# Kernel optimization log

Measured on AMD Instinct MI355X. Metric: run time of the kernel, lower is better.

## Reference

```python
import jax, jax.numpy as jnp
import numpy as np

B, T, D = 4, 2048, 1024
H, DH = 16, 64

def setup_inputs() -> dict:
    key = jax.random.key(0)
    k1, k2, k3 = jax.random.split(key, 3)
    x = jax.random.normal(k1, (B, T, D), dtype=jnp.float32)
    # nn.Linear weights stored [out, in]; we keep that convention
    w_attn = jax.random.normal(k2, (3 * D, D), dtype=jnp.float32) * (1.0 / np.sqrt(D))
    w_proj = jax.random.normal(k3, (D, D), dtype=jnp.float32) * (1.0 / np.sqrt(D))
    return {"x": x, "w_attn": w_attn, "w_proj": w_proj}

def reference(x, w_attn, w_proj):
    Bx, Tx, Dx = x.shape
    qkv = jnp.einsum('btd,ed->bte', x, w_attn)            # [B,T,3D]
    qkv = qkv.reshape(Bx, Tx, 3, H, DH)
    q = qkv[:, :, 0].transpose(0, 2, 1, 3)                # [B,H,T,DH]
    k = qkv[:, :, 1].transpose(0, 2, 1, 3)
    v = qkv[:, :, 2].transpose(0, 2, 1, 3)
    scale = 1.0 / np.sqrt(DH).astype(np.float32)
    att = jnp.einsum('bhqd,bhkd->bhqk', q, k) * scale     # [B,H,T,T]
    causal = jnp.tril(jnp.ones((Tx, Tx), dtype=bool))
    att = jnp.where(causal[None, None], att, jnp.float32(-jnp.inf))
    att = jax.nn.softmax(att, axis=-1)
    y = jnp.einsum('bhqk,bhkd->bhqd', att, v)             # [B,H,T,DH]
    y = y.transpose(0, 2, 1, 3).reshape(Bx, Tx, Dx)       # [B,T,D]
    y = jnp.einsum('btd,ed->bte', y, w_proj)
    return y
```

## Files before the change

### kernel.cpp

```cpp
#include <hip/hip_runtime.h>

typedef unsigned short u16;
typedef __bf16 bf16x8 __attribute__((ext_vector_type(8)));
typedef float floatx4 __attribute__((ext_vector_type(4)));

__device__ inline u16 f2bf(float x) {
    __bf16 b = (__bf16)x;
    return __builtin_bit_cast(u16, b);
}

__device__ inline floatx4 fzero() {
    floatx4 z = {0.f, 0.f, 0.f, 0.f};
    return z;
}

#if defined(__has_builtin)
#if __has_builtin(__builtin_amdgcn_exp2f)
#define EXP2F(x) __builtin_amdgcn_exp2f(x)
#endif
#endif
#ifndef EXP2F
#define EXP2F(x) exp2f(x)
#endif

template <bool F32>
__device__ inline bf16x8 ld8(const void* base, size_t off) {
    if constexpr (F32) {
        const float* p = (const float*)base + off;
        float4 a = *(const float4*)p;
        float4 b = *(const float4*)(p + 4);
        union { u16 u[8]; bf16x8 v; } t;
        t.u[0] = f2bf(a.x); t.u[1] = f2bf(a.y); t.u[2] = f2bf(a.z); t.u[3] = f2bf(a.w);
        t.u[4] = f2bf(b.x); t.u[5] = f2bf(b.y); t.u[6] = f2bf(b.z); t.u[7] = f2bf(b.w);
        return t.v;
    } else {
        return *(const bf16x8*)((const u16*)base + off);
    }
}

typedef __attribute__((address_space(1))) const unsigned int as1_u32;
typedef __attribute__((address_space(3))) unsigned int as3_u32;
__device__ inline void gld_lds16(const void* g, void* l) {
    __builtin_amdgcn_global_load_lds((as1_u32*)g, (as3_u32*)l, 16, 0, 0);
}

__device__ inline u16* swz_ptr(u16* buf, int row, int col) {
    return (u16*)((char*)buf + row * 128 + ((col * 2) ^ ((row & 7) << 4)));
}

__global__ __launch_bounds__(256) void cvt_all(const float* __restrict__ x,
                                               const float* __restrict__ wa,
                                               const float* __restrict__ wp,
                                               u16* __restrict__ dst) {
    const int XB8 = 1048576, WAB8 = 393216;
    int i = blockIdx.x * 256 + threadIdx.x;
    const float* src; size_t off;
    if (i < XB8)             { src = x;  off = (size_t)i * 8; }
    else if (i < XB8 + WAB8) { src = wa; off = (size_t)(i - XB8) * 8; }
    else                     { src = wp; off = (size_t)(i - XB8 - WAB8) * 8; }
    *(bf16x8*)(dst + (size_t)i * 8) = ld8<true>(src, off);
}

#define BK 32

template <bool AF32, bool BF32, bool CF32>
__global__ __launch_bounds__(256) void gemm_bt(const void* __restrict__ Ap,
                                               const void* __restrict__ Bp,
                                               void* __restrict__ Cp,
                                               int M, int N, int K) {
    __shared__ alignas(16) u16 As[2][128 * BK];
    __shared__ alignas(16) u16 Bs[2][128 * BK];

    const int tid  = threadIdx.x;
    const int lane = tid & 63;
    const int wave = tid >> 6;
    const int wm = (wave >> 1) * 64;
    const int wn = (wave & 1) * 64;
    const int tm = blockIdx.y * 128;
    const int tn = blockIdx.x * 128;
    const int l15 = lane & 15;
    const int l4  = lane >> 4;

    const int srow = tid >> 2;
    const int scol = (tid & 3) * 8;

    floatx4 acc[4][4];
#pragma unroll
    for (int i = 0; i < 4; i++)
#pragma unroll
        for (int j = 0; j < 4; j++) acc[i][j] = fzero();

    if constexpr (!AF32 && !BF32) {
        const u16* Ag = (const u16*)Ap + (size_t)(tm + srow) * K + scol;
        const u16* Bg = (const u16*)Bp + (size_t)(tn + srow) * K + scol;

        auto stage = [&](int buf, int k0) {
            gld_lds16(Ag + k0,                  &As[buf][wave * 512]);
            gld_lds16(Ag + k0 + (size_t)64 * K, &As[buf][2048 + wave * 512]);
            gld_lds16(Bg + k0,                  &Bs[buf][wave * 512]);
            gld_lds16(Bg + k0 + (size_t)64 * K, &Bs[buf][2048 + wave * 512]);
        };

        stage(0, 0);
        __syncthreads();
        int cur = 0;
        const int nk = K / BK;
        for (int t = 0; t < nk; t++) {
            if (t + 1 < nk) stage(cur ^ 1, (t + 1) * BK);

            bf16x8 af[4], bfv[4];
#pragma unroll
            for (int i = 0; i < 4; i++)
                af[i] = *(const bf16x8*)&As[cur][(wm + i * 16 + l15) * BK + l4 * 8];
#pragma unroll
            for (int j = 0; j < 4; j++)
                bfv[j] = *(const bf16x8*)&Bs[cur][(wn + j * 16 + l15) * BK + l4 * 8];
#pragma unroll
            for (int i = 0; i < 4; i++)
#pragma unroll
                for (int j = 0; j < 4; j++)
                    acc[i][j] = __builtin_amdgcn_mfma_f32_16x16x32_bf16(af[i], bfv[j], acc[i][j], 0, 0, 0);

            __syncthreads();
            cur ^= 1;
        }
    } else {
        for (int k0 = 0; k0 < K; k0 += BK) {
            bf16x8 av[2], bv[2];
#pragma unroll
            for (int q = 0; q < 2; q++) {
                av[q] = ld8<AF32>(Ap, (size_t)(tm + srow + q * 64) * K + k0 + scol);
                bv[q] = ld8<BF32>(Bp, (size_t)(tn + srow + q * 64) * K + k0 + scol);
            }
            __syncthreads();
#pragma unroll
            for (int q = 0; q < 2; q++) {
                *(bf16x8*)&As[0][(srow + q * 64) * BK + scol] = av[q];
                *(bf16x8*)&Bs[0][(srow + q * 64) * BK + scol] = bv[q];
            }
            __syncthreads();

            bf16x8 af[4], bfv[4];
#pragma unroll
            for (int i = 0; i < 4; i++)
                af[i] = *(const bf16x8*)&As[0][(wm + i * 16 + l15) * BK + l4 * 8];
#pragma unroll
            for (int j = 0; j < 4; j++)
                bfv[j] = *(const bf16x8*)&Bs[0][(wn + j * 16 + l15) * BK + l4 * 8];
#pragma unroll
            for (int i = 0; i < 4; i++)
#pragma unroll
                for (int j = 0; j < 4; j++)
                    acc[i][j] = __builtin_amdgcn_mfma_f32_16x16x32_bf16(af[i], bfv[j], acc[i][j], 0, 0, 0);
        }
    }

#pragma unroll
    for (int i = 0; i < 4; i++)
#pragma unroll
        for (int j = 0; j < 4; j++)
#pragma unroll
            for (int r = 0; r < 4; r++) {
                int row = tm + wm + i * 16 + l4 * 4 + r;
                int col = tn + wn + j * 16 + l15;
                if constexpr (CF32)
                    ((float*)Cp)[(size_t)row * N + col] = acc[i][j][r];
                else
                    ((u16*)Cp)[(size_t)row * N + col] = f2bf(acc[i][j][r]);
            }
}

__global__ __launch_bounds__(256) void attn2(const u16* __restrict__ qkv,
                                             u16* __restrict__ y) {
    const int T = 2048, CW = 3072;
    __shared__ alignas(16) u16 Kb[2][64 * 64];
    __shared__ alignas(16) u16 Vb[2][64 * 64];
    __shared__ alignas(16) u16 PB[64 * 64];

    const int tid  = threadIdx.x;
    const int lane = tid & 63;
    const int wave = tid >> 6;
    const int l15 = lane & 15;
    const int l4  = lane >> 4;

    const int bh = blockIdx.x;
    const int qt = 31 - blockIdx.y;
    const int b = bh >> 4, h = bh & 15;
    const int q0 = qt * 64;

    const size_t base = (size_t)b * T * CW + h * 64;
    const u16* qp = qkv + base;
    const u16* kp = qkv + base + 1024;
    const u16* vp = qkv + base + 2048;

    bf16x8 qf[2];
    {
        int qrow = q0 + wave * 16 + l15;
        qf[0] = *(const bf16x8*)&qp[(size_t)qrow * CW + l4 * 8];
        qf[1] = *(const bf16x8*)&qp[(size_t)qrow * CW + 32 + l4 * 8];
    }

    bf16x8 ones;
#pragma unroll
    for (int i = 0; i < 8; i++) ones[i] = (__bf16)1.0f;

    const float C2 = 0.18033688f;
    floatx4 Lacc = fzero();
    floatx4 Oacc[4];
#pragma unroll
    for (int cf = 0; cf < 4; cf++) Oacc[cf] = fzero();

    const int sr = tid >> 3;
    const int sc = tid & 7;
    const int dh = lane;
    const int tb = wave * 8;

    bf16x8 kreg[2], vreg[2];
    auto stage_load = [&](int kt) {
        const int t0 = kt * 64;
#pragma unroll
        for (int p = 0; p < 2; p++)
            kreg[p] = *(const bf16x8*)&kp[(size_t)(t0 + sr + p * 32) * CW + sc * 8];
#pragma unroll
        for (int p = 0; p < 2; p++) {
            union { u16 u[8]; bf16x8 v; } tmp;
#pragma unroll
            for (int i = 0; i < 8; i++)
                tmp.u[i] = vp[(size_t)(t0 + tb + p * 32 + i) * CW + dh];
            vreg[p] = tmp.v;
        }
    };

    auto commit = [&](int buf) {
#pragma unroll
        for (int p = 0; p < 2; p++)
            *(bf16x8*)swz_ptr(&Kb[buf][0], sr + p * 32, sc * 8) = kreg[p];
#pragma unroll
        for (int p = 0; p < 2; p++)
            *(bf16x8*)swz_ptr(&Vb[buf][0], dh, tb + p * 32) = vreg[p];
    };

    stage_load(0);
    commit(0);
    if (qt >= 1) stage_load(1);
    __syncthreads();

    for (int kt = 0; kt <= qt; kt++) {
        const int t0 = kt * 64;
        const int cur = kt & 1;
        u16* KP = &Kb[cur][0];
        u16* Vt = &Vb[cur][0];

#pragma unroll
        for (int j = 0; j < 4; j++) {
            bf16x8 k0f = *(const bf16x8*)swz_ptr(KP, j * 16 + l15, l4 * 8);
            bf16x8 k1f = *(const bf16x8*)swz_ptr(KP, j * 16 + l15, 32 + l4 * 8);
            floatx4 s = fzero();
            s = __builtin_amdgcn_mfma_f32_16x16x32_bf16(qf[0], k0f, s, 0, 0, 0);
            s = __builtin_amdgcn_mfma_f32_16x16x32_bf16(qf[1], k1f, s, 0, 0, 0);
            float pj[4];
            if (kt == qt) {
#pragma unroll
                for (int r = 0; r < 4; r++) {
                    int qrow = q0 + wave * 16 + l4 * 4 + r;
                    int krow = t0 + j * 16 + l15;
                    float e = (krow <= qrow) ? s[r] * C2 : -1.0e30f;
                    pj[r] = EXP2F(e);
                }
            } else {
#pragma unroll
                for (int r = 0; r < 4; r++) pj[r] = EXP2F(s[r] * C2);
            }
#pragma unroll
            for (int r = 0; r < 4; r++)
                *swz_ptr(PB, wave * 16 + l4 * 4 + r, j * 16 + l15) = f2bf(pj[r]);
        }

        bf16x8 pf0 = *(const bf16x8*)swz_ptr(PB, wave * 16 + l15, l4 * 8);
        bf16x8 pf1 = *(const bf16x8*)swz_ptr(PB, wave * 16 + l15, 32 + l4 * 8);
        Lacc = __builtin_amdgcn_mfma_f32_16x16x32_bf16(pf0, ones, Lacc, 0, 0, 0);
        Lacc = __builtin_amdgcn_mfma_f32_16x16x32_bf16(pf1, ones, Lacc, 0, 0, 0);
#pragma unroll
        for (int cf = 0; cf < 4; cf++) {
            bf16x8 v0f = *(const bf16x8*)swz_ptr(Vt, cf * 16 + l15, l4 * 8);
            bf16x8 v1f = *(const bf16x8*)swz_ptr(Vt, cf * 16 + l15, 32 + l4 * 8);
            Oacc[cf] = __builtin_amdgcn_mfma_f32_16x16x32_bf16(pf0, v0f, Oacc[cf], 0, 0, 0);
            Oacc[cf] = __builtin_amdgcn_mfma_f32_16x16x32_bf16(pf1, v1f, Oacc[cf], 0, 0, 0);
        }

        if (kt + 1 <= qt) commit(cur ^ 1);
        if (kt + 2 <= qt) stage_load(kt + 2);
        __syncthreads();
    }

#pragma unroll
    for (int r = 0; r < 4; r++) {
        float inv = 1.0f / Lacc[r];
        int qrow = q0 + wave * 16 + l4 * 4 + r;
        size_t orow = ((size_t)b * T + qrow) * 1024 + h * 64;
#pragma unroll
        for (int cf = 0; cf < 4; cf++)
            y[orow + cf * 16 + l15] = f2bf(Oacc[cf][r] * inv);
    }
}

extern "C" void kernel_launch(void* const* d_in, const int* in_sizes, int n_in,
                              void* d_out, int out_size, void* d_ws, size_t ws_size,
                              hipStream_t stream) {
    const float* x      = (const float*)d_in[0];
    const float* w_attn = (const float*)d_in[1];
    const float* w_proj = (const float*)d_in[2];
    float* out = (float*)d_out;

    const size_t QKV = (size_t)8192 * 3072;
    const size_t Y   = (size_t)8192 * 1024;
    const size_t XB  = (size_t)8192 * 1024;
    const size_t WAB = (size_t)3072 * 1024;
    const size_t WPB = (size_t)1024 * 1024;

    u16* qkv = (u16*)d_ws;
    u16* yb  = qkv + QKV;

    const bool full = ws_size >= (QKV + Y + XB + WAB + WPB) * sizeof(u16);
    if (ws_size < (QKV + Y) * sizeof(u16)) return;

    dim3 blk(256);
    dim3 g1(3072 / 128, 8192 / 128), g2(1024 / 128, 8192 / 128);
    dim3 ga(64, 32);

    if (full) {
        u16* xb  = yb + Y;
        cvt_all<<<6144, blk, 0, stream>>>(x, w_attn, w_proj, xb);
        u16* wab = xb + XB;
        u16* wpb = wab + WAB;
        gemm_bt<false, false, false><<<g1, blk, 0, stream>>>(xb, wab, qkv, 8192, 3072, 1024);
        attn2<<<ga, blk, 0, stream>>>(qkv, yb);
        gemm_bt<false, false, true><<<g2, blk, 0, stream>>>(yb, wpb, out, 8192, 1024, 1024);
    } else {
        gemm_bt<true, true, false><<<g1, blk, 0, stream>>>(x, w_attn, qkv, 8192, 3072, 1024);
        attn2<<<ga, blk, 0, stream>>>(qkv, yb);
        gemm_bt<false, true, true><<<g2, blk, 0, stream>>>(yb, w_proj, out, 8192, 1024, 1024);
    }
}
```

Baseline: 251.3 us.

## Stage V tiles via direct global-to-LDS loads and transpose within LDS

V tiles were previously gathered from global memory with strided 2-byte loads, one element per row, to build the transposed layout. Now V rows are copied into a double-buffered raw LDS area with coalesced 16-byte global-to-LDS loads, then transposed LDS-to-LDS into the swizzled Vt buffer. K becomes single-buffered, and the loop needs an extra barrier per iteration. This trades uncoalesced global traffic for added LDS reads and writes and more synchronisation.

Result: slower. 274.0 us (+9.0%).

```diff
diff --git a/kernel.cpp b/kernel.cpp
--- a/kernel.cpp
+++ b/kernel.cpp
@@ -173,8 +173,9 @@
 __global__ __launch_bounds__(256) void attn2(const u16* __restrict__ qkv,
                                              u16* __restrict__ y) {
     const int T = 2048, CW = 3072;
-    __shared__ alignas(16) u16 Kb[2][64 * 64];
-    __shared__ alignas(16) u16 Vb[2][64 * 64];
+    __shared__ alignas(16) u16 KP[64 * 64];
+    __shared__ alignas(16) u16 Vr[2][64 * 64];
+    __shared__ alignas(16) u16 Vt[64 * 64];
     __shared__ alignas(16) u16 PB[64 * 64];
 
     const int tid  = threadIdx.x;
@@ -212,44 +213,49 @@
 
     const int sr = tid >> 3;
     const int sc = tid & 7;
-    const int dh = lane;
     const int tb = wave * 8;
 
-    bf16x8 kreg[2], vreg[2];
-    auto stage_load = [&](int kt) {
+    bf16x8 kreg[2];
+    auto kload = [&](int kt) {
         const int t0 = kt * 64;
 #pragma unroll
         for (int p = 0; p < 2; p++)
             kreg[p] = *(const bf16x8*)&kp[(size_t)(t0 + sr + p * 32) * CW + sc * 8];
+    };
+    auto vstage = [&](int buf, int kt) {
+        const int t0 = kt * 64;
+#pragma unroll
+        for (int p = 0; p < 2; p++)
+            gld_lds16(&vp[(size_t)(t0 + sr + p * 32) * CW + sc * 8],
+                      &Vr[buf][p * 2048 + wave * 512]);
+    };
+    auto kcommit = [&]() {
+#pragma unroll
+        for (int p = 0; p < 2; p++)
+            *(bf16x8*)swz_ptr(KP, sr + p * 32, sc * 8) = kreg[p];
+    };
+    auto vtrans = [&](int buf) {
+        const u16* vr = &Vr[buf][0];
 #pragma unroll
         for (int p = 0; p < 2; p++) {
-            union { u16 u[8]; bf16x8 v; } tmp;
+            union { u16 u[8]; bf16x8 v; } t;
 #pragma unroll
             for (int i = 0; i < 8; i++)
-                tmp.u[i] = vp[(size_t)(t0 + tb + p * 32 + i) * CW + dh];
-            vreg[p] = tmp.v;
+                t.u[i] = vr[(tb + p * 32 + i) * 64 + lane];
+            *(bf16x8*)swz_ptr(Vt, lane, tb + p * 32) = t.v;
         }
     };
 
-    auto commit = [&](int buf) {
-#pragma unroll
-        for (int p = 0; p < 2; p++)
-            *(bf16x8*)swz_ptr(&Kb[buf][0], sr + p * 32, sc * 8) = kreg[p];
-#pragma unroll
-        for (int p = 0; p < 2; p++)
-            *(bf16x8*)swz_ptr(&Vb[buf][0], dh, tb + p * 32) = vreg[p];
-    };
-
-    stage_load(0);
-    commit(0);
-    if (qt >= 1) stage_load(1);
+    kload(0);
+    vstage(0, 0);
+    __syncthreads();
+    kcommit();
+    vtrans(0);
+    if (qt >= 1) { kload(1); vstage(1, 1); }
     __syncthreads();
 
     for (int kt = 0; kt <= qt; kt++) {
         const int t0 = kt * 64;
-        const int cur = kt & 1;
-        u16* KP = &Kb[cur][0];
-        u16* Vt = &Vb[cur][0];
 
 #pragma unroll
         for (int j = 0; j < 4; j++) {
@@ -288,9 +294,16 @@
             Oacc[cf] = __builtin_amdgcn_mfma_f32_16x16x32_bf16(pf1, v1f, Oacc[cf], 0, 0, 0);
         }
 
-        if (kt + 1 <= qt) commit(cur ^ 1);
-        if (kt + 2 <= qt) stage_load(kt + 2);
+        if (kt == qt) break;
+
         __syncthreads();
+        kcommit();
+        vtrans((kt + 1) & 1);
+        __syncthreads();
+        if (kt + 2 <= qt) {
+            kload(kt + 2);
+            vstage(kt & 1, kt + 2);
+        }
     }
 
 #pragma unroll
```
